# Kernel optimization log

Hardware: AMD Instinct MI355X
Metric: run time of the kernel (lower is better)

## Reference

```python
import jax, jax.numpy as jnp
import numpy as np

DIM, HEADS, DFF = 768, 12, 3072
DK = DIM // HEADS
EPS = 1e-5

def _layernorm(x, w, b):
    mu = jnp.mean(x, axis=-1, keepdims=True)
    var = jnp.mean(jnp.square(x - mu), axis=-1, keepdims=True)
    return (x - mu) * jax.lax.rsqrt(var + EPS) * w + b

def setup_inputs() -> dict:
    key = jax.random.key(0)
    ks = jax.random.split(key, 5)
    B, N = 8, 1024
    std = 0.02
    return {
        "x": jax.random.normal(ks[0], (B, N, DIM), jnp.float32),
        "ln1_w": jnp.ones((DIM,), jnp.float32),
        "ln1_b": jnp.zeros((DIM,), jnp.float32),
        "qkv_w": jax.random.normal(ks[1], (3 * DIM, DIM), jnp.float32) * std,
        "qkv_b": jnp.zeros((3 * DIM,), jnp.float32),
        "proj_w": jax.random.normal(ks[2], (DIM, DIM), jnp.float32) * std,
        "proj_b": jnp.zeros((DIM,), jnp.float32),
        "ln2_w": jnp.ones((DIM,), jnp.float32),
        "ln2_b": jnp.zeros((DIM,), jnp.float32),
        "fc1_w": jax.random.normal(ks[3], (DFF, DIM), jnp.float32) * std,
        "fc1_b": jnp.zeros((DFF,), jnp.float32),
        "fc2_w": jax.random.normal(ks[4], (DIM, DFF), jnp.float32) * std,
        "fc2_b": jnp.zeros((DIM,), jnp.float32),
    }

def reference(x, ln1_w, ln1_b, qkv_w, qkv_b, proj_w, proj_b,
              ln2_w, ln2_b, fc1_w, fc1_b, fc2_w, fc2_b):
    B, N, C = x.shape
    # --- attention branch (pre-norm) ---
    h = _layernorm(x, ln1_w, ln1_b)
    qkv = h @ qkv_w.T + qkv_b                      # [B,N,3C]
    qkv = qkv.reshape(B, N, 3, HEADS, DK)
    q = qkv[:, :, 0].transpose(0, 2, 1, 3)         # [B,H,N,dk]
    k = qkv[:, :, 1].transpose(0, 2, 1, 3)
    v = qkv[:, :, 2].transpose(0, 2, 1, 3)
    scale = DK ** -0.5
    attn = jnp.einsum('bhnd,bhmd->bhnm', q, k) * scale
    attn = jax.nn.softmax(attn, axis=-1)
    out = jnp.einsum('bhnm,bhmd->bhnd', attn, v)   # [B,H,N,dk]
    out = out.transpose(0, 2, 1, 3).reshape(B, N, C)
    out = out @ proj_w.T + proj_b
    x = x + out
    # --- MLP branch (pre-norm) ---
    h = _layernorm(x, ln2_w, ln2_b)
    h = jax.nn.gelu(h @ fc1_w.T + fc1_b, approximate=False)
    h = h @ fc2_w.T + fc2_b
    return x + h
```

## Files before the change

kernel.cpp:

```cpp
#include <hip/hip_runtime.h>
#include <hip/hip_bf16.h>
#include <hip/hip_fp8.h>
#include <math.h>

typedef __attribute__((ext_vector_type(8))) __bf16 bf16x8;
typedef __attribute__((ext_vector_type(4))) __bf16 bf16x4;
typedef __attribute__((ext_vector_type(4))) float f32x4;
typedef __attribute__((ext_vector_type(4))) int i32x4;
typedef __attribute__((ext_vector_type(8))) int i32x8;

#define DIM 768
#define DFF 3072
#define HEADS 12
#define DKH 64
#define SEQ 1024
#define BATCH 8
#define ROWS (SEQ * BATCH)

#define GLD16(gp, lp)                                                      \
  __builtin_amdgcn_global_load_lds(                                        \
      (const __attribute__((address_space(1))) void*)(gp),                 \
      (__attribute__((address_space(3))) void*)(lp), 16, 0, 0)

__device__ __forceinline__ unsigned int pack4_e4m3(float a, float b, float c, float d) {
  __hip_fp8_e4m3 q0(a), q1(b), q2(c), q3(d);
  return (unsigned int)q0.__x | ((unsigned int)q1.__x << 8) |
         ((unsigned int)q2.__x << 16) | ((unsigned int)q3.__x << 24);
}

__global__ __launch_bounds__(256) void cvt4_kernel(const float* __restrict__ s0, int n0,
                                                   const float* __restrict__ s1, int n1,
                                                   const float* __restrict__ s2, int n2,
                                                   const float* __restrict__ s3, int n3,
                                                   __bf16* __restrict__ d0,
                                                   __bf16* __restrict__ d1,
                                                   unsigned char* __restrict__ d2,
                                                   unsigned char* __restrict__ d3) {
  int i0 = blockIdx.x * 256 + threadIdx.x;
  int st = gridDim.x * 256;
  const float* bsrc[2] = {s0, s1};
  __bf16* bdst[2] = {d0, d1};
  int bns[2] = {n0, n1};
#pragma unroll
  for (int t = 0; t < 2; ++t) {
    const f32x4* in = reinterpret_cast<const f32x4*>(bsrc[t]);
    bf16x4* out = reinterpret_cast<bf16x4*>(bdst[t]);
    for (int i = i0; i < bns[t]; i += st) {
      f32x4 v = in[i];
      bf16x4 o;
#pragma unroll
      for (int j = 0; j < 4; ++j) o[j] = (__bf16)v[j];
      out[i] = o;
    }
  }
  const float* fsrc[2] = {s2, s3};
  unsigned char* fdst[2] = {d2, d3};
  int fns[2] = {n2, n3};
#pragma unroll
  for (int t = 0; t < 2; ++t) {
    const f32x4* in = reinterpret_cast<const f32x4*>(fsrc[t]);
    unsigned int* out = reinterpret_cast<unsigned int*>(fdst[t]);
    for (int i = i0; i < fns[t]; i += st) {
      f32x4 v = in[i];
      out[i] = pack4_e4m3(v[0] * 16.f, v[1] * 16.f, v[2] * 16.f, v[3] * 16.f);
    }
  }
}

__global__ __launch_bounds__(256) void ln_kernel(const float* __restrict__ x,
                                                 const float* __restrict__ w,
                                                 const float* __restrict__ b,
                                                 __bf16* __restrict__ out) {
  int wid = threadIdx.x >> 6, lane = threadIdx.x & 63;
  int row = blockIdx.x * 4 + wid;
  const f32x4* xp = reinterpret_cast<const f32x4*>(x + (size_t)row * DIM);
  f32x4 v[3];
  float s1 = 0.f, s2 = 0.f;
#pragma unroll
  for (int i = 0; i < 3; ++i) {
    v[i] = xp[lane + i * 64];
#pragma unroll
    for (int c = 0; c < 4; ++c) { s1 += v[i][c]; s2 += v[i][c] * v[i][c]; }
  }
#pragma unroll
  for (int off = 1; off < 64; off <<= 1) {
    s1 += __shfl_xor(s1, off, 64);
    s2 += __shfl_xor(s2, off, 64);
  }
  float mu = s1 * (1.f / DIM);
  float var = s2 * (1.f / DIM) - mu * mu;
  float rs = rsqrtf(var + 1e-5f);
  const f32x4* wp = reinterpret_cast<const f32x4*>(w);
  const f32x4* bp = reinterpret_cast<const f32x4*>(b);
  __bf16* op = out + (size_t)row * DIM;
#pragma unroll
  for (int i = 0; i < 3; ++i) {
    int c4 = lane + i * 64;
    f32x4 wv = wp[c4], bv = bp[c4];
    bf16x4 ov;
#pragma unroll
    for (int c = 0; c < 4; ++c) ov[c] = (__bf16)((v[i][c] - mu) * rs * wv[c] + bv[c]);
    *reinterpret_cast<bf16x4*>(&op[c4 * 4]) = ov;
  }
}

__global__ __launch_bounds__(256) void ln_f8_kernel(const float* __restrict__ x,
                                                    const float* __restrict__ w,
                                                    const float* __restrict__ b,
                                                    unsigned char* __restrict__ out) {
  int wid = threadIdx.x >> 6, lane = threadIdx.x & 63;
  int row = blockIdx.x * 4 + wid;
  const f32x4* xp = reinterpret_cast<const f32x4*>(x + (size_t)row * DIM);
  f32x4 v[3];
  float s1 = 0.f, s2 = 0.f;
#pragma unroll
  for (int i = 0; i < 3; ++i) {
    v[i] = xp[lane + i * 64];
#pragma unroll
    for (int c = 0; c < 4; ++c) { s1 += v[i][c]; s2 += v[i][c] * v[i][c]; }
  }
#pragma unroll
  for (int off = 1; off < 64; off <<= 1) {
    s1 += __shfl_xor(s1, off, 64);
    s2 += __shfl_xor(s2, off, 64);
  }
  float mu = s1 * (1.f / DIM);
  float var = s2 * (1.f / DIM) - mu * mu;
  float rs = rsqrtf(var + 1e-5f);
  const f32x4* wp = reinterpret_cast<const f32x4*>(w);
  const f32x4* bp = reinterpret_cast<const f32x4*>(b);
  unsigned int* op = reinterpret_cast<unsigned int*>(out + (size_t)row * DIM);
#pragma unroll
  for (int i = 0; i < 3; ++i) {
    int c4 = lane + i * 64;
    f32x4 wv = wp[c4], bv = bp[c4];
    float o0 = (v[i][0] - mu) * rs * wv[0] + bv[0];
    float o1 = (v[i][1] - mu) * rs * wv[1] + bv[1];
    float o2 = (v[i][2] - mu) * rs * wv[2] + bv[2];
    float o3 = (v[i][3] - mu) * rs * wv[3] + bv[3];
    op[c4] = pack4_e4m3(o0, o1, o2, o3);
  }
}

template <int EPI>
__global__ __launch_bounds__(512, 4) void gemm_nt(const __bf16* __restrict__ A,
                                                  const __bf16* __restrict__ B,
                                                  const float* __restrict__ bias,
                                                  const float* __restrict__ resid,
                                                  __bf16* __restrict__ vt,
                                                  void* __restrict__ Cout,
                                                  int M, int N, int K) {
  __shared__ __bf16 As[2 * 128 * 64];
  __shared__ __bf16 Bs[2 * 128 * 64];
  int tid = threadIdx.x;
  int bm = blockIdx.x, bn = blockIdx.y;
  int wid = tid >> 6, lane = tid & 63;
  int l15 = lane & 15, l4 = lane >> 4;
  int rowb = (wid >> 1) * 32;
  int colb = (wid & 1) * 64;

  f32x4 acc[2][4] = {};

  auto stage = [&](int buf, int kt) {
    __bf16* Ab = As + buf * 128 * 64;
    __bf16* Bb = Bs + buf * 128 * 64;
#pragma unroll
    for (int r = 0; r < 2; ++r) {
      int c0 = (r * 8 + wid) * 64;
      int c = c0 + lane;
      int row = c >> 3;
      int colE = ((c & 7) ^ (row & 7)) * 8;
      GLD16(&A[(size_t)(bm * 128 + row) * K + kt + colE], &Ab[c0 * 8]);
    }
#pragma unroll
    for (int r = 0; r < 2; ++r) {
      int c0 = (r * 8 + wid) * 64;
      int c = c0 + lane;
      int row = c >> 3;
      int colE = ((c & 7) ^ (row & 7)) * 8;
      GLD16(&B[(size_t)(bn * 128 + row) * K + kt + colE], &Bb[c0 * 8]);
    }
  };

  auto compute = [&](int buf) {
    const __bf16* Ab = As + buf * 128 * 64;
    const __bf16* Bb = Bs + buf * 128 * 64;
#pragma unroll
    for (int kc = 0; kc < 2; ++kc) {
      int cswz = ((kc * 4 + l4) ^ (l15 & 7)) * 8;
      bf16x8 af[2], bfr[4];
#pragma unroll
      for (int m = 0; m < 2; ++m)
        af[m] = *reinterpret_cast<const bf16x8*>(&Ab[(rowb + m * 16 + l15) * 64 + cswz]);
#pragma unroll
      for (int n = 0; n < 4; ++n)
        bfr[n] = *reinterpret_cast<const bf16x8*>(&Bb[(colb + n * 16 + l15) * 64 + cswz]);
#pragma unroll
      for (int m = 0; m < 2; ++m)
#pragma unroll
        for (int n = 0; n < 4; ++n)
          acc[m][n] = __builtin_amdgcn_mfma_f32_16x16x32_bf16(af[m], bfr[n], acc[m][n], 0, 0, 0);
    }
  };

  stage(0, 0);
  int cur = 0;
  for (int kt = 0; kt < K; kt += 64) {
    if (kt + 64 < K) {
      stage(cur ^ 1, kt + 64);
      asm volatile("s_waitcnt vmcnt(4)" ::: "memory");
    } else {
      asm volatile("s_waitcnt vmcnt(0)" ::: "memory");
    }
    __builtin_amdgcn_s_barrier();
    compute(cur);
    asm volatile("s_waitcnt lgkmcnt(0)" ::: "memory");
    __builtin_amdgcn_s_barrier();
    cur ^= 1;
  }

#pragma unroll
  for (int m = 0; m < 2; ++m)
#pragma unroll
    for (int n = 0; n < 4; ++n) {
      int row0 = bm * 128 + rowb + m * 16 + l4 * 4;
      int col = bn * 128 + colb + n * 16 + l15;
      float bc = bias[col];
      if (EPI == 0 && col >= 2 * DIM) {
        int h = (col - 2 * DIM) >> 6, dk = (col - 2 * DIM) & 63;
        int b = row0 >> 10, tok = row0 & 1023;
        bf16x4 pk;
#pragma unroll
        for (int j = 0; j < 4; ++j) pk[j] = (__bf16)(acc[m][n][j] + bc);
        *reinterpret_cast<bf16x4*>(
            &vt[(size_t)((b * HEADS + h) * DKH + dk) * SEQ + tok]) = pk;
      } else {
#pragma unroll
        for (int j = 0; j < 4; ++j) {
          float v = acc[m][n][j] + bc;
          size_t idx = (size_t)(row0 + j) * N + col;
          if (EPI == 0) {
            ((__bf16*)Cout)[idx] = (__bf16)v;
          } else {
            ((float*)Cout)[idx] = v + resid[idx];
          }
        }
      }
    }
}

template <int EPI>
__global__ __launch_bounds__(512, 4) void gemm_fp8(const unsigned char* __restrict__ A,
                                                   const unsigned char* __restrict__ B,
                                                   const float* __restrict__ bias,
                                                   const float* __restrict__ resid,
                                                   void* __restrict__ Cout,
                                                   int M, int N, int K) {
  __shared__ unsigned char As[2 * 128 * 128];
  __shared__ unsigned char Bs[2 * 128 * 128];
  int tid = threadIdx.x;
  int bm = blockIdx.x, bn = blockIdx.y;
  int wid = tid >> 6, lane = tid & 63;
  int l15 = lane & 15, l4 = lane >> 4;
  int rowb = (wid >> 1) * 32;
  int colb = (wid & 1) * 64;

  f32x4 acc[2][4] = {};

  auto stage = [&](int buf, int kt) {
    unsigned char* Ab = As + buf * 128 * 128;
    unsigned char* Bb = Bs + buf * 128 * 128;
#pragma unroll
    for (int r = 0; r < 2; ++r) {
      int c0 = (r * 8 + wid) * 64;
      int c = c0 + lane;
      int row = c >> 3;
      int j = (c & 7) ^ (row & 7);
      GLD16(&A[(size_t)(bm * 128 + row) * K + kt + j * 16], &Ab[c0 * 16]);
    }
#pragma unroll
    for (int r = 0; r < 2; ++r) {
      int c0 = (r * 8 + wid) * 64;
      int c = c0 + lane;
      int row = c >> 3;
      int j = (c & 7) ^ (row & 7);
      GLD16(&B[(size_t)(bn * 128 + row) * K + kt + j * 16], &Bb[c0 * 16]);
    }
  };

  auto ld32 = [&](const unsigned char* base, int row) -> i32x8 {
    int s7 = l15 & 7;
    i32x8 r;
    *reinterpret_cast<i32x4*>(&r) =
        *reinterpret_cast<const i32x4*>(&base[row * 128 + (((2 * l4) ^ s7) * 16)]);
    *(reinterpret_cast<i32x4*>(&r) + 1) =
        *reinterpret_cast<const i32x4*>(&base[row * 128 + (((2 * l4 + 1) ^ s7) * 16)]);
    return r;
  };

  auto compute = [&](int buf) {
    const unsigned char* Ab = As + buf * 128 * 128;
    const unsigned char* Bb = Bs + buf * 128 * 128;
    i32x8 af[2], bfr[4];
#pragma unroll
    for (int m = 0; m < 2; ++m) af[m] = ld32(Ab, rowb + m * 16 + l15);
#pragma unroll
    for (int n = 0; n < 4; ++n) bfr[n] = ld32(Bb, colb + n * 16 + l15);
#pragma unroll
    for (int m = 0; m < 2; ++m)
#pragma unroll
      for (int n = 0; n < 4; ++n)
        acc[m][n] = __builtin_amdgcn_mfma_scale_f32_16x16x128_f8f6f4(
            af[m], bfr[n], acc[m][n], 0, 0,
            0, 0x7F7F7F7F,
            0, 0x7F7F7F7F);
  };

  stage(0, 0);
  int cur = 0;
  for (int kt = 0; kt < K; kt += 128) {
    if (kt + 128 < K) {
      stage(cur ^ 1, kt + 128);
      asm volatile("s_waitcnt vmcnt(4)" ::: "memory");
    } else {
      asm volatile("s_waitcnt vmcnt(0)" ::: "memory");
    }
    __builtin_amdgcn_s_barrier();
    compute(cur);
    asm volatile("s_waitcnt lgkmcnt(0)" ::: "memory");
    __builtin_amdgcn_s_barrier();
    cur ^= 1;
  }

#pragma unroll
  for (int m = 0; m < 2; ++m)
#pragma unroll
    for (int n = 0; n < 4; ++n) {
      int row0 = bm * 128 + rowb + m * 16 + l4 * 4;
      int col = bn * 128 + colb + n * 16 + l15;
      float bc = bias[col];
#pragma unroll
      for (int j = 0; j < 4; ++j) {
        if (EPI == 0) {
          float v = acc[m][n][j] * 0.0625f + bc;
          float z = 1.59576912f * (v + 0.044715f * v * v * v);
          float tt = __expf(fminf(z, 80.f));
          float g = v * __fdividef(tt, tt + 1.0f);
          ((unsigned char*)Cout)[(size_t)(row0 + j) * N + col] =
              __hip_fp8_e4m3(g * 16.f).__x;
        } else {
          size_t idx = (size_t)(row0 + j) * N + col;
          ((float*)Cout)[idx] = acc[m][n][j] * (1.f / 256.f) + bc + resid[idx];
        }
      }
    }
}

__global__ __launch_bounds__(256, 3) void attn_kernel(const __bf16* __restrict__ qkv,
                                                      const __bf16* __restrict__ vt,
                                                      __bf16* __restrict__ out) {
  int bid = blockIdx.x;
  int xcd = bid & 7, kk0 = bid >> 3;
  int bh = (kk0 >> 3) * 8 + xcd;
  int qt = kk0 & 7;
  int b = bh / HEADS, h = bh % HEADS;
  int tid = threadIdx.x, wid = tid >> 6, lane = tid & 63;
  int l15 = lane & 15, l4 = lane >> 4;
  int qr0 = qt * 128 + wid * 32;
  const size_t rs = 3 * DIM;
  const __bf16* Qb = qkv + (size_t)(b * SEQ) * rs + h * DKH;
  const __bf16* Kb = Qb + DIM;
  const __bf16* Vb = vt + (size_t)bh * DKH * SEQ;

  __shared__ __bf16 Ks[64 * 64];
  __shared__ __bf16 Vs[64 * 64];
  __shared__ __bf16 Ps[4][32][72];
  __bf16(*Psw)[72] = Ps[wid];

  bf16x8 qf[2][2];
#pragma unroll
  for (int m = 0; m < 2; ++m)
#pragma unroll
    for (int kc = 0; kc < 2; ++kc) {
      bf16x8 t = *reinterpret_cast<const bf16x8*>(
          &Qb[(size_t)(qr0 + m * 16 + l15) * rs + kc * 32 + l4 * 8]);
#pragma unroll
      for (int e = 0; e < 8; ++e) t[e] = (__bf16)((float)t[e] * 0.125f);
      qf[m][kc] = t;
    }

  f32x4 o[2][4] = {};
  f32x4 lsum[2] = {};

  for (int kv0 = 0; kv0 < SEQ; kv0 += 64) {
    __syncthreads();
#pragma unroll
    for (int cc = 0; cc < 2; ++cc) {
      int c0 = (wid * 2 + cc) * 64;
      int c = c0 + lane;
      int row = c >> 3;
      int sb = (c & 7) * 16;
      int pkc = sb ^ (((row >> 2) & 7) << 4);
      GLD16(&Kb[(size_t)(kv0 + row) * rs + (pkc >> 1)], &Ks[c0 * 8]);
      int pvc = sb ^ ((row & 7) << 4);
      GLD16(&Vb[(size_t)row * SEQ + kv0 + (pvc >> 1)], &Vs[c0 * 8]);
    }
    __syncthreads();

    bf16x8 kb[4][2];
#pragma unroll
    for (int nf = 0; nf < 4; ++nf)
#pragma unroll
      for (int kc = 0; kc < 2; ++kc) {
        int row = 4 * l15 + nf;
        int col = (kc * 64 + l4 * 16) ^ ((l15 & 7) << 4);
        kb[nf][kc] = *reinterpret_cast<const bf16x8*>(&Ks[row * 64 + (col >> 1)]);
      }
    f32x4 s[2][4] = {};
#pragma unroll
    for (int m = 0; m < 2; ++m)
#pragma unroll
      for (int nf = 0; nf < 4; ++nf)
#pragma unroll
        for (int kc = 0; kc < 2; ++kc)
          s[m][nf] = __builtin_amdgcn_mfma_f32_16x16x32_bf16(qf[m][kc], kb[nf][kc], s[m][nf], 0, 0, 0);

    bf16x8 vf[4][2];
#pragma unroll
    for (int d = 0; d < 4; ++d)
#pragma unroll
      for (int kc = 0; kc < 2; ++kc) {
        int row = d * 16 + l15;
        int col = (kc * 64 + l4 * 16) ^ ((l15 & 7) << 4);
        vf[d][kc] = *reinterpret_cast<const bf16x8*>(&Vs[row * 64 + (col >> 1)]);
      }

#pragma unroll
    for (int m = 0; m < 2; ++m)
#pragma unroll
      for (int j = 0; j < 4; ++j) {
        bf16x4 pk;
        float ss = 0.f;
#pragma unroll
        for (int nf = 0; nf < 4; ++nf) {
          float p = __expf(s[m][nf][j]);
          ss += p;
          pk[nf] = (__bf16)p;
        }
        lsum[m][j] += ss;
        *reinterpret_cast<bf16x4*>(&Psw[m * 16 + l4 * 4 + j][l15 * 4]) = pk;
      }
    asm volatile("s_waitcnt lgkmcnt(0)" ::: "memory");
    __builtin_amdgcn_sched_barrier(0);

    bf16x8 pf[2][2];
#pragma unroll
    for (int m = 0; m < 2; ++m)
#pragma unroll
      for (int kc = 0; kc < 2; ++kc)
        pf[m][kc] = *reinterpret_cast<const bf16x8*>(&Psw[m * 16 + l15][kc * 32 + l4 * 8]);
#pragma unroll
    for (int m = 0; m < 2; ++m)
#pragma unroll
      for (int d = 0; d < 4; ++d)
#pragma unroll
        for (int kc = 0; kc < 2; ++kc)
          o[m][d] = __builtin_amdgcn_mfma_f32_16x16x32_bf16(pf[m][kc], vf[d][kc], o[m][d], 0, 0, 0);
  }

#pragma unroll
  for (int off = 1; off < 16; off <<= 1)
#pragma unroll
    for (int m = 0; m < 2; ++m)
#pragma unroll
      for (int j = 0; j < 4; ++j) lsum[m][j] += __shfl_xor(lsum[m][j], off, 64);

  __bf16* op = out + (size_t)(b * SEQ) * DIM + h * DKH;
#pragma unroll
  for (int m = 0; m < 2; ++m)
#pragma unroll
    for (int j = 0; j < 4; ++j) {
      float rl = 1.f / lsum[m][j];
      int row = qr0 + m * 16 + l4 * 4 + j;
#pragma unroll
      for (int d = 0; d < 4; ++d)
        op[(size_t)row * DIM + d * 16 + l15] = (__bf16)(o[m][d][j] * rl);
    }
}

extern "C" void kernel_launch(void* const* d_in, const int* in_sizes, int n_in,
                              void* d_out, int out_size, void* d_ws, size_t ws_size,
                              hipStream_t stream) {
  const float* x      = (const float*)d_in[0];
  const float* ln1_w  = (const float*)d_in[1];
  const float* ln1_b  = (const float*)d_in[2];
  const float* qkv_w  = (const float*)d_in[3];
  const float* qkv_b  = (const float*)d_in[4];
  const float* proj_w = (const float*)d_in[5];
  const float* proj_b = (const float*)d_in[6];
  const float* ln2_w  = (const float*)d_in[7];
  const float* ln2_b  = (const float*)d_in[8];
  const float* fc1_w  = (const float*)d_in[9];
  const float* fc1_b  = (const float*)d_in[10];
  const float* fc2_w  = (const float*)d_in[11];
  const float* fc2_b  = (const float*)d_in[12];

  char* ws = (char*)d_ws;
  size_t o = 0;
  __bf16* qkvw_bf = (__bf16*)(ws + o); o += (size_t)3 * DIM * DIM * 2;
  __bf16* projw_bf = (__bf16*)(ws + o); o += (size_t)DIM * DIM * 2;
  unsigned char* fc1w_f8 = (unsigned char*)(ws + o); o += (size_t)DFF * DIM;
  unsigned char* fc2w_f8 = (unsigned char*)(ws + o); o += (size_t)DIM * DFF;
  __bf16* h_bf    = (__bf16*)(ws + o); o += (size_t)ROWS * DIM * 2;
  float*  x1      = (float*)(ws + o);  o += (size_t)ROWS * DIM * 4;
  __bf16* qkv_bf  = (__bf16*)(ws + o); o += (size_t)ROWS * 3 * DIM * 2;
  __bf16* attn_bf = (__bf16*)(ws + o); o += (size_t)ROWS * DIM * 2;
  unsigned char* ff_f8 = (unsigned char*)qkv_bf;
  __bf16* vtp     = (__bf16*)x1;
  unsigned char* h_f8 = (unsigned char*)h_bf;

  cvt4_kernel<<<2048, 256, 0, stream>>>(
      qkv_w, 3 * DIM * DIM / 4, proj_w, DIM * DIM / 4,
      fc1_w, DFF * DIM / 4, fc2_w, DIM * DFF / 4,
      qkvw_bf, projw_bf, fc1w_f8, fc2w_f8);

  ln_kernel<<<ROWS / 4, 256, 0, stream>>>(x, ln1_w, ln1_b, h_bf);
  gemm_nt<0><<<dim3(ROWS / 128, 3 * DIM / 128), 512, 0, stream>>>(
      h_bf, qkvw_bf, qkv_b, nullptr, vtp, qkv_bf, ROWS, 3 * DIM, DIM);
  attn_kernel<<<dim3(8 * BATCH * HEADS), 256, 0, stream>>>(qkv_bf, vtp, attn_bf);
  gemm_nt<2><<<dim3(ROWS / 128, DIM / 128), 512, 0, stream>>>(
      attn_bf, projw_bf, proj_b, x, nullptr, x1, ROWS, DIM, DIM);
  ln_f8_kernel<<<ROWS / 4, 256, 0, stream>>>(x1, ln2_w, ln2_b, h_f8);
  gemm_fp8<0><<<dim3(ROWS / 128, DFF / 128), 512, 0, stream>>>(
      h_f8, fc1w_f8, fc1_b, nullptr, ff_f8, ROWS, DFF, DIM);
  gemm_fp8<1><<<dim3(ROWS / 128, DIM / 128), 512, 0, stream>>>(
      ff_f8, fc2w_f8, fc2_b, x1, (float*)d_out, ROWS, DIM, DFF);
}
```

Baseline: 192.3 us.

## Drop double-buffered LDS staging in GEMMs to raise occupancy

Both the bf16 and fp8 GEMM kernels move from two LDS buffers with prefetch of the next K tile to a single buffer. Each K step is now sync, load, sync, compute. Launch bounds go from 4 to 8 blocks, which halves LDS per block and tightens the register budget. The aim is more resident waves to hide latency. The cost is that global loads no longer overlap MFMA work, and register pressure may cause spills.

```diff
diff --git a/kernel.cpp b/kernel.cpp
--- a/kernel.cpp
+++ b/kernel.cpp
@@ -143,15 +143,15 @@
 }
 
 template <int EPI>
-__global__ __launch_bounds__(512, 4) void gemm_nt(const __bf16* __restrict__ A,
+__global__ __launch_bounds__(512, 8) void gemm_nt(const __bf16* __restrict__ A,
                                                   const __bf16* __restrict__ B,
                                                   const float* __restrict__ bias,
                                                   const float* __restrict__ resid,
                                                   __bf16* __restrict__ vt,
                                                   void* __restrict__ Cout,
                                                   int M, int N, int K) {
-  __shared__ __bf16 As[2 * 128 * 64];
-  __shared__ __bf16 Bs[2 * 128 * 64];
+  __shared__ __bf16 As[128 * 64];
+  __shared__ __bf16 Bs[128 * 64];
   int tid = threadIdx.x;
   int bm = blockIdx.x, bn = blockIdx.y;
   int wid = tid >> 6, lane = tid & 63;
@@ -161,16 +161,14 @@
 
   f32x4 acc[2][4] = {};
 
-  auto stage = [&](int buf, int kt) {
-    __bf16* Ab = As + buf * 128 * 64;
-    __bf16* Bb = Bs + buf * 128 * 64;
+  auto stage = [&](int kt) {
 #pragma unroll
     for (int r = 0; r < 2; ++r) {
       int c0 = (r * 8 + wid) * 64;
       int c = c0 + lane;
       int row = c >> 3;
       int colE = ((c & 7) ^ (row & 7)) * 8;
-      GLD16(&A[(size_t)(bm * 128 + row) * K + kt + colE], &Ab[c0 * 8]);
+      GLD16(&A[(size_t)(bm * 128 + row) * K + kt + colE], &As[c0 * 8]);
     }
 #pragma unroll
     for (int r = 0; r < 2; ++r) {
@@ -178,23 +176,21 @@
       int c = c0 + lane;
       int row = c >> 3;
       int colE = ((c & 7) ^ (row & 7)) * 8;
-      GLD16(&B[(size_t)(bn * 128 + row) * K + kt + colE], &Bb[c0 * 8]);
+      GLD16(&B[(size_t)(bn * 128 + row) * K + kt + colE], &Bs[c0 * 8]);
     }
   };
 
-  auto compute = [&](int buf) {
-    const __bf16* Ab = As + buf * 128 * 64;
-    const __bf16* Bb = Bs + buf * 128 * 64;
+  auto compute = [&]() {
 #pragma unroll
     for (int kc = 0; kc < 2; ++kc) {
       int cswz = ((kc * 4 + l4) ^ (l15 & 7)) * 8;
       bf16x8 af[2], bfr[4];
 #pragma unroll
       for (int m = 0; m < 2; ++m)
-        af[m] = *reinterpret_cast<const bf16x8*>(&Ab[(rowb + m * 16 + l15) * 64 + cswz]);
+        af[m] = *reinterpret_cast<const bf16x8*>(&As[(rowb + m * 16 + l15) * 64 + cswz]);
 #pragma unroll
       for (int n = 0; n < 4; ++n)
-        bfr[n] = *reinterpret_cast<const bf16x8*>(&Bb[(colb + n * 16 + l15) * 64 + cswz]);
+        bfr[n] = *reinterpret_cast<const bf16x8*>(&Bs[(colb + n * 16 + l15) * 64 + cswz]);
 #pragma unroll
       for (int m = 0; m < 2; ++m)
 #pragma unroll
@@ -203,20 +199,11 @@
     }
   };
 
-  stage(0, 0);
-  int cur = 0;
   for (int kt = 0; kt < K; kt += 64) {
-    if (kt + 64 < K) {
-      stage(cur ^ 1, kt + 64);
-      asm volatile("s_waitcnt vmcnt(4)" ::: "memory");
-    } else {
-      asm volatile("s_waitcnt vmcnt(0)" ::: "memory");
-    }
-    __builtin_amdgcn_s_barrier();
-    compute(cur);
-    asm volatile("s_waitcnt lgkmcnt(0)" ::: "memory");
-    __builtin_amdgcn_s_barrier();
-    cur ^= 1;
+    __syncthreads();
+    stage(kt);
+    __syncthreads();
+    compute();
   }
 
 #pragma unroll
@@ -250,14 +237,14 @@
 }
 
 template <int EPI>
-__global__ __launch_bounds__(512, 4) void gemm_fp8(const unsigned char* __restrict__ A,
+__global__ __launch_bounds__(512, 8) void gemm_fp8(const unsigned char* __restrict__ A,
                                                    const unsigned char* __restrict__ B,
                                                    const float* __restrict__ bias,
                                                    const float* __restrict__ resid,
                                                    void* __restrict__ Cout,
                                                    int M, int N, int K) {
-  __shared__ unsigned char As[2 * 128 * 128];
-  __shared__ unsigned char Bs[2 * 128 * 128];
+  __shared__ unsigned char As[128 * 128];
+  __shared__ unsigned char Bs[128 * 128];
   int tid = threadIdx.x;
   int bm = blockIdx.x, bn = blockIdx.y;
   int wid = tid >> 6, lane = tid & 63;
@@ -267,16 +254,14 @@
 
   f32x4 acc[2][4] = {};
 
-  auto stage = [&](int buf, int kt) {
-    unsigned char* Ab = As + buf * 128 * 128;
-    unsigned char* Bb = Bs + buf * 128 * 128;
+  auto stage = [&](int kt) {
 #pragma unroll
     for (int r = 0; r < 2; ++r) {
       int c0 = (r * 8 + wid) * 64;
       int c = c0 + lane;
       int row = c >> 3;
       int j = (c & 7) ^ (row & 7);
-      GLD16(&A[(size_t)(bm * 128 + row) * K + kt + j * 16], &Ab[c0 * 16]);
+      GLD16(&A[(size_t)(bm * 128 + row) * K + kt + j * 16], &As[c0 * 16]);
     }
 #pragma unroll
     for (int r = 0; r < 2; ++r) {
@@ -284,7 +269,7 @@
       int c = c0 + lane;
       int row = c >> 3;
       int j = (c & 7) ^ (row & 7);
-      GLD16(&B[(size_t)(bn * 128 + row) * K + kt + j * 16], &Bb[c0 * 16]);
+      GLD16(&B[(size_t)(bn * 128 + row) * K + kt + j * 16], &Bs[c0 * 16]);
     }
   };
 
@@ -298,14 +283,12 @@
     return r;
   };
 
-  auto compute = [&](int buf) {
-    const unsigned char* Ab = As + buf * 128 * 128;
-    const unsigned char* Bb = Bs + buf * 128 * 128;
+  auto compute = [&]() {
     i32x8 af[2], bfr[4];
 #pragma unroll
-    for (int m = 0; m < 2; ++m) af[m] = ld32(Ab, rowb + m * 16 + l15);
-#pragma unroll
-    for (int n = 0; n < 4; ++n) bfr[n] = ld32(Bb, colb + n * 16 + l15);
+    for (int m = 0; m < 2; ++m) af[m] = ld32(As, rowb + m * 16 + l15);
+#pragma unroll
+    for (int n = 0; n < 4; ++n) bfr[n] = ld32(Bs, colb + n * 16 + l15);
 #pragma unroll
     for (int m = 0; m < 2; ++m)
 #pragma unroll
@@ -316,20 +299,11 @@
             0, 0x7F7F7F7F);
   };
 
-  stage(0, 0);
-  int cur = 0;
   for (int kt = 0; kt < K; kt += 128) {
-    if (kt + 128 < K) {
-      stage(cur ^ 1, kt + 128);
-      asm volatile("s_waitcnt vmcnt(4)" ::: "memory");
-    } else {
-      asm volatile("s_waitcnt vmcnt(0)" ::: "memory");
-    }
-    __builtin_amdgcn_s_barrier();
-    compute(cur);
-    asm volatile("s_waitcnt lgkmcnt(0)" ::: "memory");
-    __builtin_amdgcn_s_barrier();
-    cur ^= 1;
+    __syncthreads();
+    stage(kt);
+    __syncthreads();
+    compute();
   }
 
 #pragma unroll
```

Measured after the change: 409.6 us. +113.0%, slower.
